# Kernel optimization log

Hardware: AMD Instinct MI355X
Metric: run time of the kernel (lower is better)

Reference implementation:

```python
import jax, jax.numpy as jnp
import numpy as np

D_MODEL = 1024
N_HEADS = 16
D_K = D_MODEL // N_HEADS


def setup_inputs() -> dict:
    key = jax.random.key(0)
    ks = jax.random.split(key, 9)
    B, L = 2, 2048
    s = 1.0 / np.sqrt(D_MODEL)
    return {
        "x": jax.random.normal(ks[0], (B, L, D_MODEL), dtype=jnp.float32),
        "Wq": jax.random.normal(ks[1], (D_MODEL, D_MODEL), dtype=jnp.float32) * s,
        "bq": jnp.zeros((D_MODEL,), dtype=jnp.float32),
        "Wk": jax.random.normal(ks[2], (D_MODEL, D_MODEL), dtype=jnp.float32) * s,
        "bk": jnp.zeros((D_MODEL,), dtype=jnp.float32),
        "Wv": jax.random.normal(ks[3], (D_MODEL, D_MODEL), dtype=jnp.float32) * s,
        "bv": jnp.zeros((D_MODEL,), dtype=jnp.float32),
        "Wo": jax.random.normal(ks[4], (D_MODEL, D_MODEL), dtype=jnp.float32) * s,
        "bo": jnp.zeros((D_MODEL,), dtype=jnp.float32),
    }


def reference(x, Wq, bq, Wk, bk, Wv, bv, Wo, bo):
    B, L, D = x.shape
    H, dk = N_HEADS, D_K
    # torch Linear: y = x @ W.T + b
    def proj(W, b):
        y = jnp.einsum('bld,ed->ble', x, W) + b
        return y.reshape(B, L, H, dk).transpose(0, 2, 1, 3)  # [B,H,L,dk]
    Q = proj(Wq, bq)
    K = proj(Wk, bk)
    V = proj(Wv, bv)
    scores = jnp.einsum('bhqd,bhkd->bhqk', Q, K) / jnp.sqrt(jnp.float32(dk))
    probs = jax.nn.softmax(scores, axis=-1)
    # intervention: zero column 0, then average with original -> halve column 0
    col_scale = jnp.where(jnp.arange(L) == 0, 0.5, 1.0).astype(probs.dtype)
    combined = probs * col_scale  # broadcast over last axis
    out = jnp.einsum('bhqk,bhkd->bhqd', combined, V)
    out = out.transpose(0, 2, 1, 3).reshape(B, L, D)
    # dropout in eval mode = identity
    return jnp.einsum('bld,ed->ble', out, Wo) + bo
```

## Files before the change

### kernel.cpp

```cpp
#include <hip/hip_runtime.h>
#include <stdint.h>

#define DMODEL 1024
#define LSEQ   2048
#define NBATCH 2
#define NHEADS 16
#define DKH    64
#define MROWS  4096
#define KSPLIT 2

typedef __attribute__((ext_vector_type(8))) short short8;
typedef __attribute__((ext_vector_type(4))) float f32x4;
typedef __attribute__((ext_vector_type(16))) float f32x16;
typedef __attribute__((ext_vector_type(2))) int int2v;

__device__ __forceinline__ unsigned short f2b(float f) {
  union { float f; unsigned int u; } v; v.f = f;
  unsigned int r = v.u + 0x7FFFu + ((v.u >> 16) & 1u);
  return (unsigned short)(r >> 16);
}

__device__ __forceinline__ float b2f(unsigned short u) {
  union { unsigned int i; float f; } v; v.i = ((unsigned int)u) << 16; return v.f;
}

__device__ __forceinline__ unsigned int cvtpk(float lo, float hi) {
  unsigned int r;
  asm volatile("v_cvt_pk_bf16_f32 %0, %1, %2" : "=v"(r) : "v"(lo), "v"(hi));
  return r;
}

__device__ __forceinline__ int2v pl32swap(unsigned int a, unsigned int b) {
  return __builtin_amdgcn_permlane32_swap((int)a, (int)b, false, false);
}

__device__ __forceinline__ void async16(const void* g, void* l) {
  __builtin_amdgcn_global_load_lds(
      (const __attribute__((address_space(1))) unsigned int*)g,
      (__attribute__((address_space(3))) unsigned int*)l, 16, 0, 0);
}

__global__ void k_cvtall(const float* __restrict__ x,
                         const float* __restrict__ w0, const float* __restrict__ w1,
                         const float* __restrict__ w2, const float* __restrict__ w3,
                         unsigned short* __restrict__ xb,
                         unsigned short* __restrict__ d0, unsigned short* __restrict__ d1,
                         unsigned short* __restrict__ d2, unsigned short* __restrict__ d3) {
  const int y = blockIdx.y;
  const float* s; unsigned short* d;
  switch (y) {
    case 0: case 1: case 2: case 3:
      s = x + (size_t)y * 1048576; d = xb + (size_t)y * 1048576; break;
    case 4: s = w0; d = d0; break;
    case 5: s = w1; d = d1; break;
    case 6: s = w2; d = d2; break;
    default: s = w3; d = d3; break;
  }
  const int i = blockIdx.x * blockDim.x + threadIdx.x;
  float4 v = ((const float4*)s)[i];
  ushort4 o;
  o.x = f2b(v.x); o.y = f2b(v.y); o.z = f2b(v.z); o.w = f2b(v.w);
  ((ushort4*)d)[i] = o;
}

__device__ __forceinline__ void gemm_mainloop(
    const unsigned short* __restrict__ A, const unsigned short* __restrict__ B,
    int rowBase, int colBase, char* As, char* Bs, f32x4 acc[4][4])
{
  const int tid  = threadIdx.x;
  const int lane = tid & 63;
  const int wr   = tid >> 7;
  const int wc   = (tid >> 6) & 1;
  for (int kt = 0; kt < DMODEL / 64; ++kt) {
    const int k0 = kt * 64;
    __syncthreads();
#pragma unroll
    for (int p = 0; p < 4; ++p) {
      const int chunk = p * 256 + tid;
      const int row   = chunk >> 3;
      const int cs    = (chunk & 7) ^ (row & 7);
      async16(A + (size_t)(rowBase + row) * DMODEL + k0 + cs * 8,
              As + (p * 256 + (tid & 0xC0)) * 16);
      async16(B + (size_t)(colBase + row) * DMODEL + k0 + cs * 8,
              Bs + (p * 256 + (tid & 0xC0)) * 16);
    }
    __syncthreads();
#pragma unroll
    for (int ks = 0; ks < 2; ++ks) {
      short8 af[4], bfr[4];
#pragma unroll
      for (int m = 0; m < 4; ++m) {
        const int ra = wr * 64 + m * 16 + (lane & 15);
        af[m]  = *(const short8*)(As + ra * 128 + (((ks * 4 + (lane >> 4)) ^ (ra & 7)) * 16));
        const int rb = wc * 64 + m * 16 + (lane & 15);
        bfr[m] = *(const short8*)(Bs + rb * 128 + (((ks * 4 + (lane >> 4)) ^ (rb & 7)) * 16));
      }
#pragma unroll
      for (int m = 0; m < 4; ++m)
#pragma unroll
        for (int n = 0; n < 4; ++n)
          acc[m][n] = __builtin_amdgcn_mfma_f32_16x16x32_bf16(af[m], bfr[n], acc[m][n], 0, 0, 0);
    }
  }
}

__global__ __launch_bounds__(256, 2) void k_gemm_qkv(
    const unsigned short* __restrict__ xb,
    const unsigned short* __restrict__ Wqb, const unsigned short* __restrict__ Wkb,
    const unsigned short* __restrict__ Wvb,
    const float* __restrict__ bq, const float* __restrict__ bk, const float* __restrict__ bv,
    unsigned short* __restrict__ Q, unsigned short* __restrict__ Ksw,
    unsigned short* __restrict__ Vsw)
{
  __shared__ char As[16384];
  __shared__ char Bs[16384];
  const int z = blockIdx.z;
  const unsigned short* W = (z == 0) ? Wqb : ((z == 1) ? Wkb : Wvb);
  const float* bias       = (z == 0) ? bq  : ((z == 1) ? bk  : bv);
  const int rowBase = blockIdx.x * 128, colBase = blockIdx.y * 128;

  f32x4 zero = {0.f, 0.f, 0.f, 0.f};
  f32x4 acc[4][4];
#pragma unroll
  for (int m = 0; m < 4; ++m)
#pragma unroll
    for (int n = 0; n < 4; ++n) acc[m][n] = zero;

  gemm_mainloop(xb, W, rowBase, colBase, As, Bs, acc);

  const int tid = threadIdx.x, lane = tid & 63;
  const int wr = tid >> 7, wc = (tid >> 6) & 1;
  const float scale = (z == 0) ? 0.18033688011112042f : 1.0f;
#pragma unroll
  for (int m = 0; m < 4; ++m) {
#pragma unroll
    for (int n = 0; n < 4; ++n) {
      const int gcol = colBase + wc * 64 + n * 16 + (lane & 15);
      const float bb = bias[gcol];
      const int h = gcol >> 6, d = gcol & 63;
      if (z == 0) {
#pragma unroll
        for (int r = 0; r < 4; ++r) {
          const int grow = rowBase + wr * 64 + m * 16 + ((lane >> 4) << 2) + r;
          const int bi = grow >> 11, l = grow & 2047;
          Q[(((size_t)(bi * NHEADS + h)) * LSEQ + l) * DKH + d] =
              f2b((acc[m][n][r] + bb) * scale);
        }
      } else if (z == 1) {
#pragma unroll
        for (int r = 0; r < 4; ++r) {
          const int grow = rowBase + wr * 64 + m * 16 + ((lane >> 4) << 2) + r;
          const int bi = grow >> 11, l = grow & 2047;
          const int bh = bi * NHEADS + h;
          Ksw[(size_t)(bh * 32 + (l >> 6)) * 4096 + ((d >> 3) * 64 + (l & 63)) * 8 + (d & 7)] =
              f2b(acc[m][n][r] + bb);
        }
      } else {
        const int grow0 = rowBase + wr * 64 + m * 16 + ((lane >> 4) << 2);
        const int bi = grow0 >> 11, l0 = grow0 & 2047;
        const int bh = bi * NHEADS + h;
        ushort4 o;
        o.x = f2b(acc[m][n][0] + bb);
        o.y = f2b(acc[m][n][1] + bb);
        o.z = f2b(acc[m][n][2] + bb);
        o.w = f2b(acc[m][n][3] + bb);
        *(ushort4*)(Vsw + (size_t)(bh * 32 + (l0 >> 6)) * 4096 +
                    (((l0 & 63) >> 3) * 64 + d) * 8 + (l0 & 7)) = o;
      }
    }
  }
}

__global__ __launch_bounds__(256, 2) void k_attn(
    const unsigned short* __restrict__ Q, const unsigned short* __restrict__ Ksw,
    const unsigned short* __restrict__ Vsw,
    unsigned short* __restrict__ Op0, unsigned short* __restrict__ Op1,
    float* __restrict__ Lp)
{
  const int tid = threadIdx.x, lane = tid & 63;
  const int hi = lane >> 5;
  const int ql = lane & 31;
  const int w = tid >> 6;

  const int flat = blockIdx.x;
  const int g  = flat & 63;
  const int qi = flat >> 6;
  const int bh = g >> 1, ks = g & 1;
  const int b = bh >> 4, h = bh & 15;
  const int q0 = qi * 128 + w * 32;

  unsigned short* __restrict__ Op = ks ? Op1 : Op0;
  const unsigned short* __restrict__ Qh = Q + (size_t)bh * LSEQ * DKH;

  short8 qf[4];
#pragma unroll
  for (int c = 0; c < 4; ++c)
    qf[c] = *(const short8*)(Qh + (size_t)(q0 + ql) * DKH + c * 16 + hi * 8);

  union { unsigned short u[8]; short8 v; } ones;
#pragma unroll
  for (int j = 0; j < 8; ++j) ones.u[j] = 0x3F80;

  f32x16 oacc[2], lacc, z16;
#pragma unroll
  for (int r = 0; r < 16; ++r) {
    oacc[0][r] = 0.f; oacc[1][r] = 0.f; lacc[r] = 0.f; z16[r] = 0.f;
  }
  float p0 = 0.f;

  const int t0 = ks * (LSEQ / 64 / KSPLIT);
  const int NT = LSEQ / 64 / KSPLIT;

  const int lv = hi * 512 + ql * 8;
#define FOFF(c, b2) ((c) * 1024 + (b2) * 256 + lv)

  const unsigned short* Kt = Ksw + (size_t)(bh * 32 + t0) * 4096;
  const unsigned short* Vt = Vsw + (size_t)(bh * 32 + t0) * 4096;

  short8 kreg[8], vreg[8];
#pragma unroll
  for (int c = 0; c < 4; ++c)
#pragma unroll
    for (int b2 = 0; b2 < 2; ++b2) {
      kreg[c * 2 + b2] = *(const short8*)(Kt + FOFF(c, b2));
      vreg[c * 2 + b2] = *(const short8*)(Vt + FOFF(c, b2));
    }

  for (int i = 0; i < NT; ++i) {
    const unsigned short* Kn = Ksw + (size_t)(bh * 32 + t0 + i + 1) * 4096;
    const unsigned short* Vn = Vsw + (size_t)(bh * 32 + t0 + i + 1) * 4096;

    f32x16 sv[2];
#pragma unroll
    for (int c = 0; c < 4; ++c) {
      sv[0] = __builtin_amdgcn_mfma_f32_32x32x16_bf16(kreg[c * 2 + 0], qf[c],
                                                      c ? sv[0] : z16, 0, 0, 0);
      sv[1] = __builtin_amdgcn_mfma_f32_32x32x16_bf16(kreg[c * 2 + 1], qf[c],
                                                      c ? sv[1] : z16, 0, 0, 0);
    }

    if (i < NT - 1) {
#pragma unroll
      for (int c = 0; c < 4; ++c)
#pragma unroll
        for (int b2 = 0; b2 < 2; ++b2)
          kreg[c * 2 + b2] = *(const short8*)(Kn + FOFF(c, b2));
    }

#pragma unroll
    for (int b2 = 0; b2 < 2; ++b2)
#pragma unroll
      for (int r = 0; r < 16; ++r) sv[b2][r] = __builtin_amdgcn_exp2f(sv[b2][r]);

    if (ks == 0 && i == 0 && hi == 0) { p0 = sv[0][0]; sv[0][0] *= 0.5f; }

    unsigned int pk[2][4][2];
#pragma unroll
    for (int b2 = 0; b2 < 2; ++b2)
#pragma unroll
      for (int R = 0; R < 4; ++R) {
        pk[b2][R][0] = cvtpk(sv[b2][4 * R + 0], sv[b2][4 * R + 1]);
        pk[b2][R][1] = cvtpk(sv[b2][4 * R + 2], sv[b2][4 * R + 3]);
      }

#pragma unroll
    for (int kc = 0; kc < 4; ++kc) {
      const int b2 = kc >> 1, Rl = 2 * (kc & 1);
      int2v sw0 = pl32swap(pk[b2][Rl][0], pk[b2][Rl + 1][0]);
      int2v sw1 = pl32swap(pk[b2][Rl][1], pk[b2][Rl + 1][1]);
      union { int i[4]; short8 v; } pa;
      pa.i[0] = sw0[0]; pa.i[1] = sw1[0]; pa.i[2] = sw0[1]; pa.i[3] = sw1[1];
      lacc = __builtin_amdgcn_mfma_f32_32x32x16_bf16(pa.v, ones.v, lacc, 0, 0, 0);
      oacc[0] = __builtin_amdgcn_mfma_f32_32x32x16_bf16(pa.v, vreg[kc * 2 + 0], oacc[0], 0, 0, 0);
      oacc[1] = __builtin_amdgcn_mfma_f32_32x32x16_bf16(pa.v, vreg[kc * 2 + 1], oacc[1], 0, 0, 0);
    }

    if (i < NT - 1) {
#pragma unroll
      for (int c = 0; c < 4; ++c)
#pragma unroll
        for (int b2 = 0; b2 < 2; ++b2)
          vreg[c * 2 + b2] = *(const short8*)(Vn + FOFF(c, b2));
    }
  }
#undef FOFF

#pragma unroll
  for (int r = 0; r < 16; ++r) {
    const int qrow = (r & 3) + 8 * (r >> 2) + 4 * hi;
    float lv2 = lacc[r];
    if (ks == 0) lv2 += 0.5f * __shfl(p0, qrow);
#pragma unroll
    for (int n = 0; n < 2; ++n) {
      Op[(size_t)(b * LSEQ + q0 + qrow) * DMODEL + h * 64 + n * 32 + ql] =
          f2b(oacc[n][r]);
    }
    if (ql == 0)
      Lp[ks * (32 * LSEQ) + bh * LSEQ + q0 + qrow] = lv2;
  }
}

__global__ void k_combine(const unsigned short* __restrict__ o0,
                          const unsigned short* __restrict__ o1,
                          const float* __restrict__ Lp,
                          unsigned short* __restrict__ AO)
{
  const int i = blockIdx.x * blockDim.x + threadIdx.x;
  const int row = i >> 7;
  const int q = row & 2047, b = row >> 11;
  const int h = (i & 127) >> 3;
  const int bhq = (b * 16 + h) * 2048 + q;
  const float inv = 1.0f / (Lp[bhq] + Lp[32 * LSEQ + bhq]);
  short8 a = ((const short8*)o0)[i];
  short8 c = ((const short8*)o1)[i];
  union { unsigned short u[8]; short8 v; } o;
#pragma unroll
  for (int j = 0; j < 8; ++j)
    o.u[j] = f2b((b2f((unsigned short)a[j]) + b2f((unsigned short)c[j])) * inv);
  ((short8*)AO)[i] = o.v;
}

__global__ __launch_bounds__(256, 2) void k_gemm_out(
    const unsigned short* __restrict__ AO, const unsigned short* __restrict__ Wob,
    const float* __restrict__ bo, float* __restrict__ out)
{
  __shared__ char As[16384];
  __shared__ char Bs[16384];
  const int rowBase = blockIdx.x * 128, colBase = blockIdx.y * 128;
  f32x4 zero = {0.f, 0.f, 0.f, 0.f};
  f32x4 acc[4][4];
#pragma unroll
  for (int m = 0; m < 4; ++m)
#pragma unroll
    for (int n = 0; n < 4; ++n) acc[m][n] = zero;

  gemm_mainloop(AO, Wob, rowBase, colBase, As, Bs, acc);

  const int tid = threadIdx.x, lane = tid & 63;
  const int wr = tid >> 7, wc = (tid >> 6) & 1;
#pragma unroll
  for (int m = 0; m < 4; ++m) {
#pragma unroll
    for (int n = 0; n < 4; ++n) {
      const int gcol = colBase + wc * 64 + n * 16 + (lane & 15);
      const float bb = bo[gcol];
#pragma unroll
      for (int r = 0; r < 4; ++r) {
        const int grow = rowBase + wr * 64 + m * 16 + ((lane >> 4) << 2) + r;
        out[(size_t)grow * DMODEL + gcol] = acc[m][n][r] + bb;
      }
    }
  }
}

extern "C" void kernel_launch(void* const* d_in, const int* in_sizes, int n_in,
                              void* d_out, int out_size, void* d_ws, size_t ws_size,
                              hipStream_t stream) {
  const float* x  = (const float*)d_in[0];
  const float* Wq = (const float*)d_in[1];
  const float* bq = (const float*)d_in[2];
  const float* Wk = (const float*)d_in[3];
  const float* bk = (const float*)d_in[4];
  const float* Wv = (const float*)d_in[5];
  const float* bv = (const float*)d_in[6];
  const float* Wo = (const float*)d_in[7];
  const float* bo = (const float*)d_in[8];
  float* out = (float*)d_out;
  char* ws = (char*)d_ws;

  const size_t MB = 1u << 20;
  unsigned short* xb  = (unsigned short*)(ws);
  unsigned short* Wob = (unsigned short*)(ws + 8  * MB);
  unsigned short* Wqb = (unsigned short*)(ws + 10 * MB);
  unsigned short* Wkb = (unsigned short*)(ws + 12 * MB);
  unsigned short* Wvb = (unsigned short*)(ws + 14 * MB);
  unsigned short* Qb  = (unsigned short*)(ws + 16 * MB);
  unsigned short* Ksw = (unsigned short*)(ws + 24 * MB);
  unsigned short* Vsw = (unsigned short*)(ws + 32 * MB);
  unsigned short* AOb = (unsigned short*)(ws + 40 * MB);
  unsigned short* Op0 = (unsigned short*)(ws);
  unsigned short* Op1 = (unsigned short*)(ws + 48 * MB);
  float*          Lpp = (float*)(ws + 56 * MB);

  dim3 gcv(1024, 8);
  k_cvtall<<<gcv, 256, 0, stream>>>(x, Wq, Wk, Wv, Wo, xb, Wqb, Wkb, Wvb, Wob);

  dim3 gqkv(MROWS / 128, DMODEL / 128, 3);
  k_gemm_qkv<<<gqkv, 256, 0, stream>>>(xb, Wqb, Wkb, Wvb, bq, bk, bv, Qb, Ksw, Vsw);

  k_attn<<<16 * 32 * KSPLIT, 256, 0, stream>>>(Qb, Ksw, Vsw, Op0, Op1, Lpp);

  k_combine<<<2048, 256, 0, stream>>>(Op0, Op1, Lpp, AOb);

  dim3 gout(MROWS / 128, DMODEL / 128);
  k_gemm_out<<<gout, 256, 0, stream>>>(AOb, Wob, bo, out);
}
```

Before: 117.1 us.

## Software-pipeline attention loop: overlap PV MFMAs of previous tile with current QK

Restructures the attention inner loop into a prologue, steady state and epilogue. Each iteration now issues the QK^T MFMAs for tile i together with the PV and row-sum MFMAs for tile i-1, using packed probabilities held in registers (paP). The goal is to hide the exp2/convert/permute latency and the load latency behind independent matrix work. The cost is extra registers for the staged probabilities, which could reduce occupancy or cause spills.

```diff
diff --git a/kernel.cpp b/kernel.cpp
--- a/kernel.cpp
+++ b/kernel.cpp
@@ -213,23 +213,20 @@
 
   const int lv = hi * 512 + ql * 8;
 #define FOFF(c, b2) ((c) * 1024 + (b2) * 256 + lv)
-
-  const unsigned short* Kt = Ksw + (size_t)(bh * 32 + t0) * 4096;
-  const unsigned short* Vt = Vsw + (size_t)(bh * 32 + t0) * 4096;
-
-  short8 kreg[8], vreg[8];
+#define KT(t) (Ksw + (size_t)(bh * 32 + (t)) * 4096)
+#define VT(t) (Vsw + (size_t)(bh * 32 + (t)) * 4096)
+
+  short8 kreg[8], vreg[8], paP[4];
+
 #pragma unroll
   for (int c = 0; c < 4; ++c)
 #pragma unroll
     for (int b2 = 0; b2 < 2; ++b2) {
-      kreg[c * 2 + b2] = *(const short8*)(Kt + FOFF(c, b2));
-      vreg[c * 2 + b2] = *(const short8*)(Vt + FOFF(c, b2));
-    }
-
-  for (int i = 0; i < NT; ++i) {
-    const unsigned short* Kn = Ksw + (size_t)(bh * 32 + t0 + i + 1) * 4096;
-    const unsigned short* Vn = Vsw + (size_t)(bh * 32 + t0 + i + 1) * 4096;
-
+      kreg[c * 2 + b2] = *(const short8*)(KT(t0) + FOFF(c, b2));
+      vreg[c * 2 + b2] = *(const short8*)(VT(t0) + FOFF(c, b2));
+    }
+
+  {
     f32x16 sv[2];
 #pragma unroll
     for (int c = 0; c < 4; ++c) {
@@ -238,22 +235,16 @@
       sv[1] = __builtin_amdgcn_mfma_f32_32x32x16_bf16(kreg[c * 2 + 1], qf[c],
                                                       c ? sv[1] : z16, 0, 0, 0);
     }
-
-    if (i < NT - 1) {
-#pragma unroll
-      for (int c = 0; c < 4; ++c)
-#pragma unroll
-        for (int b2 = 0; b2 < 2; ++b2)
-          kreg[c * 2 + b2] = *(const short8*)(Kn + FOFF(c, b2));
-    }
-
+#pragma unroll
+    for (int c = 0; c < 4; ++c)
+#pragma unroll
+      for (int b2 = 0; b2 < 2; ++b2)
+        kreg[c * 2 + b2] = *(const short8*)(KT(t0 + 1) + FOFF(c, b2));
 #pragma unroll
     for (int b2 = 0; b2 < 2; ++b2)
 #pragma unroll
       for (int r = 0; r < 16; ++r) sv[b2][r] = __builtin_amdgcn_exp2f(sv[b2][r]);
-
-    if (ks == 0 && i == 0 && hi == 0) { p0 = sv[0][0]; sv[0][0] *= 0.5f; }
-
+    if (ks == 0 && hi == 0) { p0 = sv[0][0]; sv[0][0] *= 0.5f; }
     unsigned int pk[2][4][2];
 #pragma unroll
     for (int b2 = 0; b2 < 2; ++b2)
@@ -262,7 +253,6 @@
         pk[b2][R][0] = cvtpk(sv[b2][4 * R + 0], sv[b2][4 * R + 1]);
         pk[b2][R][1] = cvtpk(sv[b2][4 * R + 2], sv[b2][4 * R + 3]);
       }
-
 #pragma unroll
     for (int kc = 0; kc < 4; ++kc) {
       const int b2 = kc >> 1, Rl = 2 * (kc & 1);
@@ -270,9 +260,24 @@
       int2v sw1 = pl32swap(pk[b2][Rl][1], pk[b2][Rl + 1][1]);
       union { int i[4]; short8 v; } pa;
       pa.i[0] = sw0[0]; pa.i[1] = sw1[0]; pa.i[2] = sw0[1]; pa.i[3] = sw1[1];
-      lacc = __builtin_amdgcn_mfma_f32_32x32x16_bf16(pa.v, ones.v, lacc, 0, 0, 0);
-      oacc[0] = __builtin_amdgcn_mfma_f32_32x32x16_bf16(pa.v, vreg[kc * 2 + 0], oacc[0], 0, 0, 0);
-      oacc[1] = __builtin_amdgcn_mfma_f32_32x32x16_bf16(pa.v, vreg[kc * 2 + 1], oacc[1], 0, 0, 0);
+      paP[kc] = pa.v;
+    }
+  }
+
+  for (int i = 1; i < NT; ++i) {
+    f32x16 sv[2];
+#pragma unroll
+    for (int c = 0; c < 4; ++c) {
+      sv[0] = __builtin_amdgcn_mfma_f32_32x32x16_bf16(kreg[c * 2 + 0], qf[c],
+                                                      c ? sv[0] : z16, 0, 0, 0);
+      sv[1] = __builtin_amdgcn_mfma_f32_32x32x16_bf16(kreg[c * 2 + 1], qf[c],
+                                                      c ? sv[1] : z16, 0, 0, 0);
+    }
+#pragma unroll
+    for (int kc = 0; kc < 4; ++kc) {
+      lacc = __builtin_amdgcn_mfma_f32_32x32x16_bf16(paP[kc], ones.v, lacc, 0, 0, 0);
+      oacc[0] = __builtin_amdgcn_mfma_f32_32x32x16_bf16(paP[kc], vreg[kc * 2 + 0], oacc[0], 0, 0, 0);
+      oacc[1] = __builtin_amdgcn_mfma_f32_32x32x16_bf16(paP[kc], vreg[kc * 2 + 1], oacc[1], 0, 0, 0);
     }
 
     if (i < NT - 1) {
@@ -280,10 +285,46 @@
       for (int c = 0; c < 4; ++c)
 #pragma unroll
         for (int b2 = 0; b2 < 2; ++b2)
-          vreg[c * 2 + b2] = *(const short8*)(Vn + FOFF(c, b2));
-    }
+          kreg[c * 2 + b2] = *(const short8*)(KT(t0 + i + 1) + FOFF(c, b2));
+    }
+#pragma unroll
+    for (int c = 0; c < 4; ++c)
+#pragma unroll
+      for (int b2 = 0; b2 < 2; ++b2)
+        vreg[c * 2 + b2] = *(const short8*)(VT(t0 + i) + FOFF(c, b2));
+
+#pragma unroll
+    for (int b2 = 0; b2 < 2; ++b2)
+#pragma unroll
+      for (int r = 0; r < 16; ++r) sv[b2][r] = __builtin_amdgcn_exp2f(sv[b2][r]);
+    unsigned int pk[2][4][2];
+#pragma unroll
+    for (int b2 = 0; b2 < 2; ++b2)
+#pragma unroll
+      for (int R = 0; R < 4; ++R) {
+        pk[b2][R][0] = cvtpk(sv[b2][4 * R + 0], sv[b2][4 * R + 1]);
+        pk[b2][R][1] = cvtpk(sv[b2][4 * R + 2], sv[b2][4 * R + 3]);
+      }
+#pragma unroll
+    for (int kc = 0; kc < 4; ++kc) {
+      const int b2 = kc >> 1, Rl = 2 * (kc & 1);
+      int2v sw0 = pl32swap(pk[b2][Rl][0], pk[b2][Rl + 1][0]);
+      int2v sw1 = pl32swap(pk[b2][Rl][1], pk[b2][Rl + 1][1]);
+      union { int i[4]; short8 v; } pa;
+      pa.i[0] = sw0[0]; pa.i[1] = sw1[0]; pa.i[2] = sw0[1]; pa.i[3] = sw1[1];
+      paP[kc] = pa.v;
+    }
+  }
+
+#pragma unroll
+  for (int kc = 0; kc < 4; ++kc) {
+    lacc = __builtin_amdgcn_mfma_f32_32x32x16_bf16(paP[kc], ones.v, lacc, 0, 0, 0);
+    oacc[0] = __builtin_amdgcn_mfma_f32_32x32x16_bf16(paP[kc], vreg[kc * 2 + 0], oacc[0], 0, 0, 0);
+    oacc[1] = __builtin_amdgcn_mfma_f32_32x32x16_bf16(paP[kc], vreg[kc * 2 + 1], oacc[1], 0, 0, 0);
   }
 #undef FOFF
+#undef KT
+#undef VT
 
 #pragma unroll
   for (int r = 0; r < 16; ++r) {
```

Measured after the change: 122.4 us. +4.5%, slower.
